# Optimization experiments

Measured on AMD Instinct MI355X. Metric: run time of the kernel, lower is better.

## Reference

```python
import jax, jax.numpy as jnp
import numpy as np

B, T, D, H, F = 4, 2048, 512, 8, 2048
WINDOW = 128
HD = D // H
EPS = 1e-5


def layer_norm(x, g, b):
    mu = jnp.mean(x, axis=-1, keepdims=True)
    var = jnp.mean(jnp.square(x - mu), axis=-1, keepdims=True)
    return (x - mu) * jax.lax.rsqrt(var + EPS) * g + b


def setup_inputs() -> dict:
    key = jax.random.key(0)
    ks = jax.random.split(key, 5)
    s = 0.02
    return {
        "x": jax.random.normal(ks[0], (B, T, D), dtype=jnp.float32),
        "in_proj_w": jax.random.normal(ks[1], (3 * D, D), dtype=jnp.float32) * s,
        "in_proj_b": jnp.zeros((3 * D,), dtype=jnp.float32),
        "out_w": jax.random.normal(ks[2], (D, D), dtype=jnp.float32) * s,
        "out_b": jnp.zeros((D,), dtype=jnp.float32),
        "ln1_g": jnp.ones((D,), dtype=jnp.float32),
        "ln1_b": jnp.zeros((D,), dtype=jnp.float32),
        "ln2_g": jnp.ones((D,), dtype=jnp.float32),
        "ln2_b": jnp.zeros((D,), dtype=jnp.float32),
        "w1": jax.random.normal(ks[3], (F, D), dtype=jnp.float32) * s,
        "b1": jnp.zeros((F,), dtype=jnp.float32),
        "w2": jax.random.normal(ks[4], (D, F), dtype=jnp.float32) * s,
        "b2": jnp.zeros((D,), dtype=jnp.float32),
    }


def reference(x, in_proj_w, in_proj_b, out_w, out_b, ln1_g, ln1_b, ln2_g, ln2_b, w1, b1, w2, b2):
    # pre-norm sliding-window causal self-attention
    x2 = layer_norm(x, ln1_g, ln1_b)
    qkv = x2 @ in_proj_w.T + in_proj_b  # (B,T,3D)
    q, k, v = jnp.split(qkv, 3, axis=-1)
    q = q.reshape(B, T, H, HD)
    k = k.reshape(B, T, H, HD)
    v = v.reshape(B, T, H, HD)
    scale = 1.0 / np.sqrt(HD).astype(np.float32)
    scores = jnp.einsum("bthd,bshd->bhts", q, k) * scale  # dense (B,H,T,T)
    idx = jnp.arange(T)
    i = idx[:, None]
    j = idx[None, :]
    allowed = (j <= i) & (j >= i - WINDOW + 1)  # (T,T) bool, True = attend
    scores = jnp.where(allowed[None, None], scores, -jnp.inf)
    attn = jax.nn.softmax(scores, axis=-1)
    ctx = jnp.einsum("bhts,bshd->bthd", attn, v).reshape(B, T, D)
    attn_out = ctx @ out_w.T + out_b
    x = x + attn_out  # dropout is identity in eval
    # FFN block
    x3 = layer_norm(x, ln2_g, ln2_b)
    h = jax.nn.gelu(x3 @ w1.T + b1, approximate=False)
    x = x + h @ w2.T + b2
    return x
```

## Files before the change

### kernel.cpp

```cpp
#include <hip/hip_runtime.h>
#include <math.h>

constexpr int Bn = 4;
constexpr int Tn = 2048;
constexpr int Dn = 512;
constexpr int Hn = 8;
constexpr int HDn = 64;
constexpr int Fn = 2048;
constexpr int WIN = 128;
constexpr float EPS = 1e-5f;
constexpr int Mrows = Bn * Tn;
constexpr int QKVD = 3 * Dn;

using short8 = __attribute__((ext_vector_type(8))) short;
using f32x4  = __attribute__((ext_vector_type(4))) float;

__device__ __forceinline__ short f2bf(float f) {
    unsigned u = __float_as_uint(f);
    unsigned r = (u + 0x7FFFu + ((u >> 16) & 1u)) >> 16;
    return (short)r;
}

__device__ __forceinline__ float gelu_fast(float v) {
    float u = 1.5957691216f * v * (1.0f + 0.044715f * v * v);
    float t = 1.0f - 2.0f / (__expf(u) + 1.0f);
    return 0.5f * v * (1.0f + t);
}

__device__ __forceinline__ void async16(const short* g, short* l) {
    __builtin_amdgcn_global_load_lds(
        (const __attribute__((address_space(1))) void*)g,
        (__attribute__((address_space(3))) void*)l,
        16, 0, 0);
}

__global__ __launch_bounds__(256) void cvt_all(const float* __restrict__ s0,
                                               const float* __restrict__ s1,
                                               const float* __restrict__ s2,
                                               const float* __restrict__ s3,
                                               short* __restrict__ d0,
                                               short* __restrict__ d1,
                                               short* __restrict__ d2,
                                               short* __restrict__ d3)
{
    int i = blockIdx.x * 256 + threadIdx.x;
    const float* src; short* dst; int j;
    if (i < 196608)      { src = s0; dst = d0; j = i; }
    else if (i < 262144) { src = s1; dst = d1; j = i - 196608; }
    else if (i < 524288) { src = s2; dst = d2; j = i - 262144; }
    else                 { src = s3; dst = d3; j = i - 524288; }
    float4 v = ((const float4*)src)[j];
    short4 o;
    o.x = f2bf(v.x); o.y = f2bf(v.y); o.z = f2bf(v.z); o.w = f2bf(v.w);
    ((short4*)dst)[j] = o;
}

__global__ __launch_bounds__(64) void ln_kernel(const float* __restrict__ x,
                                                const float* __restrict__ g,
                                                const float* __restrict__ b,
                                                short* __restrict__ y)
{
    int row = blockIdx.x;
    int lane = threadIdx.x;
    const float4* xr = (const float4*)(x + (size_t)row * Dn);
    float4 v0 = xr[lane];
    float4 v1 = xr[lane + 64];
    float s = v0.x + v0.y + v0.z + v0.w + v1.x + v1.y + v1.z + v1.w;
#pragma unroll
    for (int off = 32; off >= 1; off >>= 1) s += __shfl_xor(s, off, 64);
    float mu = s * (1.0f / Dn);
    float d0x = v0.x - mu, d0y = v0.y - mu, d0z = v0.z - mu, d0w = v0.w - mu;
    float d1x = v1.x - mu, d1y = v1.y - mu, d1z = v1.z - mu, d1w = v1.w - mu;
    float q = d0x*d0x + d0y*d0y + d0z*d0z + d0w*d0w
            + d1x*d1x + d1y*d1y + d1z*d1z + d1w*d1w;
#pragma unroll
    for (int off = 32; off >= 1; off >>= 1) q += __shfl_xor(q, off, 64);
    float inv = rsqrtf(q * (1.0f / Dn) + EPS);
    const float4* gr = (const float4*)g;
    const float4* br = (const float4*)b;
    float4 g0 = gr[lane], g1 = gr[lane + 64];
    float4 b0 = br[lane], b1 = br[lane + 64];
    short4 a0, a1;
    a0.x = f2bf(d0x * inv * g0.x + b0.x);
    a0.y = f2bf(d0y * inv * g0.y + b0.y);
    a0.z = f2bf(d0z * inv * g0.z + b0.z);
    a0.w = f2bf(d0w * inv * g0.w + b0.w);
    a1.x = f2bf(d1x * inv * g1.x + b1.x);
    a1.y = f2bf(d1y * inv * g1.y + b1.y);
    a1.z = f2bf(d1z * inv * g1.z + b1.z);
    a1.w = f2bf(d1w * inv * g1.w + b1.w);
    short4* yr = (short4*)(y + (size_t)row * Dn);
    yr[lane] = a0;
    yr[lane + 64] = a1;
}

template <int MODE, int BK>
__global__ __launch_bounds__(256) void gemm_mfma(const short* __restrict__ A,
                                                 const short* __restrict__ Bw,
                                                 const float* __restrict__ bias,
                                                 const float* __restrict__ resid,
                                                 void* __restrict__ Cout,
                                                 short* __restrict__ q_out,
                                                 short* __restrict__ k_out,
                                                 short* __restrict__ v_out,
                                                 int M, int N, int K)
{
    constexpr int NCH = BK / 8;
    constexpr int LGN = (BK == 32) ? 2 : 3;
    constexpr int RPI = 512 / BK;
    constexpr int NI  = 32 / RPI;
    constexpr int BUF = 128 * BK;
    constexpr int KK  = BK / 32;
    __shared__ short SMEM[4 * BUF];
    short* Asb = SMEM;
    short* Bsb = SMEM + 2 * BUF;

    int tid = threadIdx.x;
    int w = tid >> 6, lane = tid & 63;
    int wr = w >> 1, wc = w & 1;
    int nN = N >> 7;
    int bid = blockIdx.x;
    int xcd = bid & 7, sq = bid >> 3;
    int mi = xcd + 8 * (sq / nN);
    int ni = sq % nN;
    int m0 = mi * 128, n0 = ni * 128;
    int quad = lane >> 4, l16 = lane & 15;

    f32x4 zero = {0.f, 0.f, 0.f, 0.f};
    f32x4 acc[4][4];
#pragma unroll
    for (int i = 0; i < 4; ++i)
#pragma unroll
        for (int j = 0; j < 4; ++j) acc[i][j] = zero;

    int rl = lane >> LGN;
    int ch = lane & (NCH - 1);
    const short* Ag[NI];
    const short* Bg[NI];
    int ldsOff[NI];
#pragma unroll
    for (int s = 0; s < NI; ++s) {
        int rowl = w * 32 + s * RPI + rl;
        int csw = (ch ^ ((rowl * BK >> 6) & (NCH - 1))) * 8;
        Ag[s] = A + (size_t)(m0 + rowl) * K + csw;
        Bg[s] = Bw + (size_t)(n0 + rowl) * K + csw;
        ldsOff[s] = (w * 32 + s * RPI) * BK;
    }

    auto stage = [&](int kt, int pp) {
#pragma unroll
        for (int s = 0; s < NI; ++s) {
            async16(Ag[s] + kt, Asb + pp * BUF + ldsOff[s]);
            async16(Bg[s] + kt, Bsb + pp * BUF + ldsOff[s]);
        }
    };

    stage(0, 0);
    int p = 0;
    for (int kt = 0; kt < K; kt += BK) {
        __syncthreads();
        if (kt + BK < K) stage(kt + BK, p ^ 1);
        short8 aF[KK][4], bF[KK][4];
#pragma unroll
        for (int kk = 0; kk < KK; ++kk)
#pragma unroll
            for (int i = 0; i < 4; ++i) {
                int ra = wr * 64 + i * 16 + l16;
                int rb = wc * 64 + i * 16 + l16;
                int cs = ((kk * 4 + quad) ^ ((ra * BK >> 6) & (NCH - 1))) * 8;
                aF[kk][i] = *(const short8*)(Asb + p * BUF + ra * BK + cs);
                bF[kk][i] = *(const short8*)(Bsb + p * BUF + rb * BK + cs);
            }
#pragma unroll
        for (int kk = 0; kk < KK; ++kk)
#pragma unroll
            for (int i = 0; i < 4; ++i)
#pragma unroll
                for (int j = 0; j < 4; ++j)
                    acc[i][j] = __builtin_amdgcn_mfma_f32_16x16x32_bf16(
                        aF[kk][i], bF[kk][j], acc[i][j], 0, 0, 0);
        p ^= 1;
    }

    if constexpr (MODE == 3) {
        __syncthreads();
        short* rp = SMEM + w * 2176;
        int b = m0 >> 11;
        int ncol0 = n0 + wc * 64;
        int sec = ncol0 >> 9;
        int h = (ncol0 & 511) >> 6;
        int bh = b * 8 + h;
        int t0 = (m0 & 2047) + wr * 64;
        if (sec == 2) {
#pragma unroll
            for (int ph = 0; ph < 2; ++ph) {
#pragma unroll
                for (int j = 2 * ph; j < 2 * ph + 2; ++j) {
                    int dl = (j - 2 * ph) * 16 + l16;
                    float bv = bias[ncol0 + j * 16 + l16];
#pragma unroll
                    for (int i = 0; i < 4; ++i)
#pragma unroll
                        for (int r = 0; r < 4; ++r)
                            rp[dl * 68 + i * 16 + quad * 4 + r] = f2bf(acc[i][j][r] + bv);
                }
#pragma unroll
                for (int it = 0; it < 4; ++it) {
                    int row = it * 8 + (lane >> 3);
                    int off = (lane & 7) * 8;
                    *(short8*)(v_out + ((size_t)bh * 64 + 32 * ph + row) * 2048 + t0 + off) =
                        *(const short8*)(rp + row * 68 + off);
                }
            }
        } else {
            short* dst = (sec == 0 ? q_out : k_out);
#pragma unroll
            for (int ph = 0; ph < 2; ++ph) {
#pragma unroll
                for (int i = 2 * ph; i < 2 * ph + 2; ++i) {
                    int tl = (i - 2 * ph) * 16 + quad * 4;
#pragma unroll
                    for (int j = 0; j < 4; ++j) {
                        float bv = bias[ncol0 + j * 16 + l16];
#pragma unroll
                        for (int r = 0; r < 4; ++r)
                            rp[(tl + r) * 68 + j * 16 + l16] = f2bf(acc[i][j][r] + bv);
                    }
                }
#pragma unroll
                for (int it = 0; it < 4; ++it) {
                    int row = it * 8 + (lane >> 3);
                    int off = (lane & 7) * 8;
                    *(short8*)(dst + ((size_t)bh * 2048 + t0 + 32 * ph + row) * 64 + off) =
                        *(const short8*)(rp + row * 68 + off);
                }
            }
        }
        return;
    }

    if constexpr (MODE == 2) {
        __syncthreads();
        short* rp = SMEM + w * 2176;
        short* Cb = (short*)Cout;
#pragma unroll
        for (int ph = 0; ph < 2; ++ph) {
#pragma unroll
            for (int i = 2 * ph; i < 2 * ph + 2; ++i) {
                int ml = (i - 2 * ph) * 16 + quad * 4;
#pragma unroll
                for (int j = 0; j < 4; ++j) {
                    float bv = bias[n0 + wc * 64 + j * 16 + l16];
#pragma unroll
                    for (int r = 0; r < 4; ++r)
                        rp[(ml + r) * 68 + j * 16 + l16] =
                            f2bf(gelu_fast(acc[i][j][r] + bv));
                }
            }
#pragma unroll
            for (int it = 0; it < 4; ++it) {
                int row = it * 8 + (lane >> 3);
                int off = (lane & 7) * 8;
                *(short8*)(Cb + (size_t)(m0 + wr * 64 + 32 * ph + row) * N
                              + n0 + wc * 64 + off) =
                    *(const short8*)(rp + row * 68 + off);
            }
        }
        return;
    }

    float* Cf = (float*)Cout;
#pragma unroll
    for (int j = 0; j < 4; ++j) {
        int n = n0 + wc * 64 + j * 16 + l16;
        float bv = bias[n];
#pragma unroll
        for (int i = 0; i < 4; ++i) {
            int mbase = m0 + wr * 64 + i * 16 + quad * 4;
#pragma unroll
            for (int r = 0; r < 4; ++r) {
                size_t idx = (size_t)(mbase + r) * N + n;
                Cf[idx] = acc[i][j][r] + bv + resid[idx];
            }
        }
    }
}

constexpr int QS = 72;
constexpr int VS = 200;

__global__ __launch_bounds__(256) void attn_mfma(const short* __restrict__ Qg,
                                                 const short* __restrict__ Kg,
                                                 const short* __restrict__ Vtg,
                                                 short* __restrict__ ctx)
{
    __shared__ short Qs[64 * QS];
    __shared__ short Ks[192 * QS];
    __shared__ short Vt[64 * VS];
    int tid = threadIdx.x;
    int w = tid >> 6, lane = tid & 63, quad = lane >> 4, l16 = lane & 15;
    int blk = blockIdx.x;
    int q0 = (blk & 31) << 6;
    int bh = blk >> 5;
    int kbase = q0 - 128;

    {
        const short* src = Qg + ((size_t)bh * 2048 + q0) * 64;
        for (int c = tid; c < 512; c += 256) {
            int row = c >> 3, off = (c & 7) * 8;
            *(short8*)(Qs + row * QS + off) = *(const short8*)(src + row * 64 + off);
        }
    }
    {
        const short* base = Kg + (size_t)bh * 2048 * 64;
        for (int c = tid; c < 1536; c += 256) {
            int row = c >> 3, off = (c & 7) * 8;
            int srow = kbase + row; srow = srow < 0 ? 0 : srow;
            *(short8*)(Ks + row * QS + off) = *(const short8*)(base + (size_t)srow * 64 + off);
        }
    }
    {
        const short* base = Vtg + (size_t)bh * 64 * 2048;
        for (int c = tid; c < 1536; c += 256) {
            int row = c / 24, cc = c - row * 24;
            int off = cc * 8;
            int scol = kbase + off; scol = scol < 0 ? 0 : scol;
            *(short8*)(Vt + row * VS + off) = *(const short8*)(base + (size_t)row * 2048 + scol);
        }
    }
    __syncthreads();

    short8 aF0 = *(const short8*)(Qs + (w * 16 + l16) * QS + quad * 8);
    short8 aF1 = *(const short8*)(Qs + (w * 16 + l16) * QS + 32 + quad * 8);
    f32x4 S[12];
    f32x4 zero = {0.f, 0.f, 0.f, 0.f};
#pragma unroll
    for (int t = 0; t < 12; ++t) S[t] = zero;
#pragma unroll
    for (int t = 0; t < 12; ++t) {
        short8 b0 = *(const short8*)(Ks + (t * 16 + l16) * QS + quad * 8);
        short8 b1 = *(const short8*)(Ks + (t * 16 + l16) * QS + 32 + quad * 8);
        S[t] = __builtin_amdgcn_mfma_f32_16x16x32_bf16(aF0, b0, S[t], 0, 0, 0);
        S[t] = __builtin_amdgcn_mfma_f32_16x16x32_bf16(aF1, b1, S[t], 0, 0, 0);
    }

    int i0 = w * 16 + quad * 4;
    float mrow[4] = {-INFINITY, -INFINITY, -INFINITY, -INFINITY};
#pragma unroll
    for (int t = 0; t < 12; ++t) {
        int jl = t * 16 + l16;
        int kg = kbase + jl;
#pragma unroll
        for (int r = 0; r < 4; ++r) {
            int dj = jl - (i0 + r);
            bool ok = (dj >= 1) && (dj <= 128) && (kg >= 0);
            float s = ok ? S[t][r] * 0.125f : -INFINITY;
            S[t][r] = s;
            mrow[r] = fmaxf(mrow[r], s);
        }
    }
#pragma unroll
    for (int off = 8; off >= 1; off >>= 1)
#pragma unroll
        for (int r = 0; r < 4; ++r)
            mrow[r] = fmaxf(mrow[r], __shfl_xor(mrow[r], off, 64));
    float sum[4] = {0.f, 0.f, 0.f, 0.f};
#pragma unroll
    for (int t = 0; t < 12; ++t)
#pragma unroll
        for (int r = 0; r < 4; ++r) {
            float p = __expf(S[t][r] - mrow[r]);
            S[t][r] = p;
            sum[r] += p;
        }
#pragma unroll
    for (int off = 8; off >= 1; off >>= 1)
#pragma unroll
        for (int r = 0; r < 4; ++r)
            sum[r] += __shfl_xor(sum[r], off, 64);
    float inv[4];
#pragma unroll
    for (int r = 0; r < 4; ++r) inv[r] = 1.0f / sum[r];

    __syncthreads();
    short* Ps = Ks;
#pragma unroll
    for (int t = 0; t < 12; ++t)
#pragma unroll
        for (int r = 0; r < 4; ++r)
            Ps[(w * 16 + quad * 4 + r) * VS + t * 16 + l16] = f2bf(S[t][r]);

    f32x4 O[4];
#pragma unroll
    for (int tN = 0; tN < 4; ++tN) O[tN] = zero;
#pragma unroll
    for (int s = 0; s < 6; ++s) {
        short8 aP = *(const short8*)(Ps + (w * 16 + l16) * VS + s * 32 + quad * 8);
#pragma unroll
        for (int tN = 0; tN < 4; ++tN) {
            short8 bV = *(const short8*)(Vt + (tN * 16 + l16) * VS + s * 32 + quad * 8);
            O[tN] = __builtin_amdgcn_mfma_f32_16x16x32_bf16(aP, bV, O[tN], 0, 0, 0);
        }
    }

    int b = bh >> 3, h = bh & 7;
#pragma unroll
    for (int tN = 0; tN < 4; ++tN)
#pragma unroll
        for (int r = 0; r < 4; ++r) {
            int trow = q0 + w * 16 + quad * 4 + r;
            ctx[((size_t)(b * 2048 + trow)) * 512 + h * 64 + tN * 16 + l16] =
                f2bf(O[tN][r] * inv[r]);
        }
}

extern "C" void kernel_launch(void* const* d_in, const int* in_sizes, int n_in,
                              void* d_out, int out_size, void* d_ws, size_t ws_size,
                              hipStream_t stream)
{
    const float* x         = (const float*)d_in[0];
    const float* in_proj_w = (const float*)d_in[1];
    const float* in_proj_b = (const float*)d_in[2];
    const float* out_w     = (const float*)d_in[3];
    const float* out_b     = (const float*)d_in[4];
    const float* ln1_g     = (const float*)d_in[5];
    const float* ln1_b     = (const float*)d_in[6];
    const float* ln2_g     = (const float*)d_in[7];
    const float* ln2_b     = (const float*)d_in[8];
    const float* w1        = (const float*)d_in[9];
    const float* b1        = (const float*)d_in[10];
    const float* w2        = (const float*)d_in[11];
    const float* b2        = (const float*)d_in[12];
    float* out = (float*)d_out;

    char* ws = (char*)d_ws;
    short* attnQ = (short*)ws;
    short* attnK = (short*)(ws + (size_t)8 * 1024 * 1024);
    short* attnV = (short*)(ws + (size_t)16 * 1024 * 1024);
    short* hbuf  = (short*)ws;
    short* regB  = (short*)(ws + (size_t)32 * 1024 * 1024);
    short* wq  = (short*)(ws + (size_t)40 * 1024 * 1024);
    short* wo  = wq + (size_t)QKVD * Dn;
    short* w1b = wo + (size_t)Dn * Dn;
    short* w2b = w1b + (size_t)Fn * Dn;

    cvt_all<<<3072, 256, 0, stream>>>(in_proj_w, out_w, w1, w2, wq, wo, w1b, w2b);

    ln_kernel<<<Mrows, 64, 0, stream>>>(x, ln1_g, ln1_b, regB);
    gemm_mfma<3, 32><<<(Mrows / 128) * (QKVD / 128), 256, 0, stream>>>(
        regB, wq, in_proj_b, nullptr, nullptr, attnQ, attnK, attnV, Mrows, QKVD, Dn);
    attn_mfma<<<Bn * Hn * (Tn / 64), 256, 0, stream>>>(attnQ, attnK, attnV, regB);
    gemm_mfma<1, 64><<<(Mrows / 128) * (Dn / 128), 256, 0, stream>>>(
        regB, wo, out_b, x, out, nullptr, nullptr, nullptr, Mrows, Dn, Dn);
    ln_kernel<<<Mrows, 64, 0, stream>>>(out, ln2_g, ln2_b, regB);
    gemm_mfma<2, 32><<<(Mrows / 128) * (Fn / 128), 256, 0, stream>>>(
        regB, w1b, b1, nullptr, hbuf, nullptr, nullptr, nullptr, Mrows, Fn, Dn);
    gemm_mfma<1, 64><<<(Mrows / 128) * (Dn / 128), 256, 0, stream>>>(
        hbuf, w2b, b2, out, out, nullptr, nullptr, nullptr, Mrows, Dn, Fn);
}
```

Before: 222.2 us.

## Use 128x256 output tiles for QKV and FFN1 GEMMs

Adds a wide GEMM kernel with 128x256 tiles (each wave computes 64x128) for the QKV projection and first FFN GEMM. The residual GEMMs move to a separate specialized 128x128 kernel. Wider tiles raise MFMA work per LDS load and halve the block count, at the cost of more accumulator registers, larger LDS, and fewer blocks in flight. The epilogues are rewritten so that each wave writes two heads for QKV.

Result: faster. 215.9 us (-2.8%).

```diff
diff --git a/kernel.cpp b/kernel.cpp
--- a/kernel.cpp
+++ b/kernel.cpp
@@ -94,23 +94,16 @@
     yr[lane + 64] = a1;
 }
 
-template <int MODE, int BK>
-__global__ __launch_bounds__(256) void gemm_mfma(const short* __restrict__ A,
-                                                 const short* __restrict__ Bw,
-                                                 const float* __restrict__ bias,
-                                                 const float* __restrict__ resid,
-                                                 void* __restrict__ Cout,
-                                                 short* __restrict__ q_out,
-                                                 short* __restrict__ k_out,
-                                                 short* __restrict__ v_out,
-                                                 int M, int N, int K)
+__global__ __launch_bounds__(256) void gemm_res(const short* __restrict__ A,
+                                                const short* __restrict__ Bw,
+                                                const float* __restrict__ bias,
+                                                const float* __restrict__ resid,
+                                                float* __restrict__ Cf,
+                                                int M, int N, int K)
 {
-    constexpr int NCH = BK / 8;
-    constexpr int LGN = (BK == 32) ? 2 : 3;
-    constexpr int RPI = 512 / BK;
-    constexpr int NI  = 32 / RPI;
+    constexpr int BK = 64;
+    constexpr int NCH = 8;
     constexpr int BUF = 128 * BK;
-    constexpr int KK  = BK / 32;
     __shared__ short SMEM[4 * BUF];
     short* Asb = SMEM;
     short* Bsb = SMEM + 2 * BUF;
@@ -133,23 +126,23 @@
 #pragma unroll
         for (int j = 0; j < 4; ++j) acc[i][j] = zero;
 
-    int rl = lane >> LGN;
-    int ch = lane & (NCH - 1);
-    const short* Ag[NI];
-    const short* Bg[NI];
-    int ldsOff[NI];
-#pragma unroll
-    for (int s = 0; s < NI; ++s) {
-        int rowl = w * 32 + s * RPI + rl;
-        int csw = (ch ^ ((rowl * BK >> 6) & (NCH - 1))) * 8;
+    int rl = lane >> 3;
+    int ch = lane & 7;
+    const short* Ag[4];
+    const short* Bg[4];
+    int ldsOff[4];
+#pragma unroll
+    for (int s = 0; s < 4; ++s) {
+        int rowl = w * 32 + s * 8 + rl;
+        int csw = (ch ^ (rowl & 7)) * 8;
         Ag[s] = A + (size_t)(m0 + rowl) * K + csw;
         Bg[s] = Bw + (size_t)(n0 + rowl) * K + csw;
-        ldsOff[s] = (w * 32 + s * RPI) * BK;
+        ldsOff[s] = (w * 32 + s * 8) * BK;
     }
 
     auto stage = [&](int kt, int pp) {
 #pragma unroll
-        for (int s = 0; s < NI; ++s) {
+        for (int s = 0; s < 4; ++s) {
             async16(Ag[s] + kt, Asb + pp * BUF + ldsOff[s]);
             async16(Bg[s] + kt, Bsb + pp * BUF + ldsOff[s]);
         }
@@ -160,19 +153,20 @@
     for (int kt = 0; kt < K; kt += BK) {
         __syncthreads();
         if (kt + BK < K) stage(kt + BK, p ^ 1);
-        short8 aF[KK][4], bF[KK][4];
-#pragma unroll
-        for (int kk = 0; kk < KK; ++kk)
+        short8 aF[2][4], bF[2][4];
+#pragma unroll
+        for (int kk = 0; kk < 2; ++kk)
 #pragma unroll
             for (int i = 0; i < 4; ++i) {
                 int ra = wr * 64 + i * 16 + l16;
                 int rb = wc * 64 + i * 16 + l16;
-                int cs = ((kk * 4 + quad) ^ ((ra * BK >> 6) & (NCH - 1))) * 8;
-                aF[kk][i] = *(const short8*)(Asb + p * BUF + ra * BK + cs);
-                bF[kk][i] = *(const short8*)(Bsb + p * BUF + rb * BK + cs);
+                int csA = ((kk * 4 + quad) ^ (ra & 7)) * 8;
+                int csB = ((kk * 4 + quad) ^ (rb & 7)) * 8;
+                aF[kk][i] = *(const short8*)(Asb + p * BUF + ra * BK + csA);
+                bF[kk][i] = *(const short8*)(Bsb + p * BUF + rb * BK + csB);
             }
 #pragma unroll
-        for (int kk = 0; kk < KK; ++kk)
+        for (int kk = 0; kk < 2; ++kk)
 #pragma unroll
             for (int i = 0; i < 4; ++i)
 #pragma unroll
@@ -182,34 +176,177 @@
         p ^= 1;
     }
 
+#pragma unroll
+    for (int j = 0; j < 4; ++j) {
+        int n = n0 + wc * 64 + j * 16 + l16;
+        float bv = bias[n];
+#pragma unroll
+        for (int i = 0; i < 4; ++i) {
+            int mbase = m0 + wr * 64 + i * 16 + quad * 4;
+#pragma unroll
+            for (int r = 0; r < 4; ++r) {
+                size_t idx = (size_t)(mbase + r) * N + n;
+                Cf[idx] = acc[i][j][r] + bv + resid[idx];
+            }
+        }
+    }
+}
+
+template <int MODE>
+__global__ __launch_bounds__(256, 2) void gemm_wide(const short* __restrict__ A,
+                                                    const short* __restrict__ Bw,
+                                                    const float* __restrict__ bias,
+                                                    void* __restrict__ Cout,
+                                                    short* __restrict__ q_out,
+                                                    short* __restrict__ k_out,
+                                                    short* __restrict__ v_out,
+                                                    int M, int N, int K)
+{
+    constexpr int BK = 32;
+    constexpr int ABUF = 128 * BK;
+    constexpr int BBUF = 256 * BK;
+    __shared__ short SMEM[2 * (ABUF + BBUF)];
+    short* Asb = SMEM;
+    short* Bsb = SMEM + 2 * ABUF;
+
+    int tid = threadIdx.x;
+    int w = tid >> 6, lane = tid & 63;
+    int wr = w >> 1, wc = w & 1;
+    int nT = N >> 8;
+    int bid = blockIdx.x;
+    int xcd = bid & 7, sq = bid >> 3;
+    int mi = xcd + 8 * (sq / nT);
+    int ni = sq % nT;
+    int m0 = mi * 128, n0 = ni * 256;
+    int quad = lane >> 4, l16 = lane & 15;
+
+    f32x4 zero = {0.f, 0.f, 0.f, 0.f};
+    f32x4 acc[4][8];
+#pragma unroll
+    for (int i = 0; i < 4; ++i)
+#pragma unroll
+        for (int j = 0; j < 8; ++j) acc[i][j] = zero;
+
+    int rl = lane >> 2;
+    int ch = lane & 3;
+    const short* Ag[2];
+    const short* Bg[4];
+    int aOff[2], bOff[4];
+#pragma unroll
+    for (int s = 0; s < 2; ++s) {
+        int rowl = w * 32 + s * 16 + rl;
+        int csw = (ch ^ ((rowl >> 1) & 3)) * 8;
+        Ag[s] = A + (size_t)(m0 + rowl) * K + csw;
+        aOff[s] = (w * 32 + s * 16) * BK;
+    }
+#pragma unroll
+    for (int s = 0; s < 4; ++s) {
+        int rowl = w * 64 + s * 16 + rl;
+        int csw = (ch ^ ((rowl >> 1) & 3)) * 8;
+        Bg[s] = Bw + (size_t)(n0 + rowl) * K + csw;
+        bOff[s] = (w * 64 + s * 16) * BK;
+    }
+
+    auto stage = [&](int kt, int pp) {
+#pragma unroll
+        for (int s = 0; s < 2; ++s)
+            async16(Ag[s] + kt, Asb + pp * ABUF + aOff[s]);
+#pragma unroll
+        for (int s = 0; s < 4; ++s)
+            async16(Bg[s] + kt, Bsb + pp * BBUF + bOff[s]);
+    };
+
+    int aoff[4], boff[8];
+#pragma unroll
+    for (int i = 0; i < 4; ++i) {
+        int ra = wr * 64 + i * 16 + l16;
+        aoff[i] = ra * BK + (quad ^ ((ra >> 1) & 3)) * 8;
+    }
+#pragma unroll
+    for (int j = 0; j < 8; ++j) {
+        int rb = wc * 128 + j * 16 + l16;
+        boff[j] = rb * BK + (quad ^ ((rb >> 1) & 3)) * 8;
+    }
+
+    stage(0, 0);
+    int p = 0;
+    for (int kt = 0; kt < K; kt += BK) {
+        __syncthreads();
+        if (kt + BK < K) stage(kt + BK, p ^ 1);
+        short8 aF[4], bF[8];
+#pragma unroll
+        for (int i = 0; i < 4; ++i)
+            aF[i] = *(const short8*)(Asb + p * ABUF + aoff[i]);
+#pragma unroll
+        for (int j = 0; j < 8; ++j)
+            bF[j] = *(const short8*)(Bsb + p * BBUF + boff[j]);
+#pragma unroll
+        for (int i = 0; i < 4; ++i)
+#pragma unroll
+            for (int j = 0; j < 8; ++j)
+                acc[i][j] = __builtin_amdgcn_mfma_f32_16x16x32_bf16(
+                    aF[i], bF[j], acc[i][j], 0, 0, 0);
+        p ^= 1;
+    }
+
+    __syncthreads();
+    short* rp = SMEM + w * 6144;
+    float bv[8];
+#pragma unroll
+    for (int j = 0; j < 8; ++j) bv[j] = bias[n0 + wc * 128 + j * 16 + l16];
+
+    if constexpr (MODE == 2) {
+        short* Cb = (short*)Cout;
+#pragma unroll
+        for (int ph = 0; ph < 2; ++ph) {
+#pragma unroll
+            for (int i = 2 * ph; i < 2 * ph + 2; ++i) {
+                int ml = (i - 2 * ph) * 16 + quad * 4;
+#pragma unroll
+                for (int j = 0; j < 8; ++j)
+#pragma unroll
+                    for (int r = 0; r < 4; ++r)
+                        rp[(ml + r) * 136 + j * 16 + l16] =
+                            f2bf(gelu_fast(acc[i][j][r] + bv[j]));
+            }
+#pragma unroll
+            for (int it = 0; it < 8; ++it) {
+                int row = it * 4 + (lane >> 4);
+                int off = (lane & 15) * 8;
+                *(short8*)(Cb + (size_t)(m0 + wr * 64 + 32 * ph + row) * N
+                              + n0 + wc * 128 + off) =
+                    *(const short8*)(rp + row * 136 + off);
+            }
+        }
+        return;
+    }
+
     if constexpr (MODE == 3) {
-        __syncthreads();
-        short* rp = SMEM + w * 2176;
         int b = m0 >> 11;
-        int ncol0 = n0 + wc * 64;
+        int ncol0 = n0 + wc * 128;
         int sec = ncol0 >> 9;
-        int h = (ncol0 & 511) >> 6;
-        int bh = b * 8 + h;
+        int h0 = (ncol0 & 511) >> 6;
         int t0 = (m0 & 2047) + wr * 64;
         if (sec == 2) {
 #pragma unroll
             for (int ph = 0; ph < 2; ++ph) {
 #pragma unroll
-                for (int j = 2 * ph; j < 2 * ph + 2; ++j) {
-                    int dl = (j - 2 * ph) * 16 + l16;
-                    float bv = bias[ncol0 + j * 16 + l16];
+                for (int j = 4 * ph; j < 4 * ph + 4; ++j) {
+                    int d = (j - 4 * ph) * 16 + l16;
 #pragma unroll
                     for (int i = 0; i < 4; ++i)
 #pragma unroll
                         for (int r = 0; r < 4; ++r)
-                            rp[dl * 68 + i * 16 + quad * 4 + r] = f2bf(acc[i][j][r] + bv);
+                            rp[d * 68 + i * 16 + quad * 4 + r] =
+                                f2bf(acc[i][j][r] + bv[j]);
                 }
-#pragma unroll
-                for (int it = 0; it < 4; ++it) {
-                    int row = it * 8 + (lane >> 3);
+                int bh = b * 8 + h0 + ph;
+#pragma unroll
+                for (int it = 0; it < 8; ++it) {
+                    int drow = it * 8 + (lane >> 3);
                     int off = (lane & 7) * 8;
-                    *(short8*)(v_out + ((size_t)bh * 64 + 32 * ph + row) * 2048 + t0 + off) =
-                        *(const short8*)(rp + row * 68 + off);
+                    *(short8*)(v_out + ((size_t)bh * 64 + drow) * 2048 + t0 + off) =
+                        *(const short8*)(rp + drow * 68 + off);
                 }
             }
         } else {
@@ -220,69 +357,24 @@
                 for (int i = 2 * ph; i < 2 * ph + 2; ++i) {
                     int tl = (i - 2 * ph) * 16 + quad * 4;
 #pragma unroll
-                    for (int j = 0; j < 4; ++j) {
-                        float bv = bias[ncol0 + j * 16 + l16];
+                    for (int j = 0; j < 8; ++j)
 #pragma unroll
                         for (int r = 0; r < 4; ++r)
-                            rp[(tl + r) * 68 + j * 16 + l16] = f2bf(acc[i][j][r] + bv);
-                    }
+                            rp[(tl + r) * 136 + j * 16 + l16] =
+                                f2bf(acc[i][j][r] + bv[j]);
                 }
 #pragma unroll
-                for (int it = 0; it < 4; ++it) {
-                    int row = it * 8 + (lane >> 3);
+                for (int it = 0; it < 8; ++it) {
+                    int trow = it * 4 + (lane >> 4);
+                    int hh = (lane & 15) >> 3;
                     int off = (lane & 7) * 8;
-                    *(short8*)(dst + ((size_t)bh * 2048 + t0 + 32 * ph + row) * 64 + off) =
-                        *(const short8*)(rp + row * 68 + off);
+                    int bh = b * 8 + h0 + hh;
+                    *(short8*)(dst + ((size_t)bh * 2048 + t0 + 32 * ph + trow) * 64 + off) =
+                        *(const short8*)(rp + trow * 136 + hh * 64 + off);
                 }
             }
         }
         return;
-    }
-
-    if constexpr (MODE == 2) {
-        __syncthreads();
-        short* rp = SMEM + w * 2176;
-        short* Cb = (short*)Cout;
-#pragma unroll
-        for (int ph = 0; ph < 2; ++ph) {
-#pragma unroll
-            for (int i = 2 * ph; i < 2 * ph + 2; ++i) {
-                int ml = (i - 2 * ph) * 16 + quad * 4;
-#pragma unroll
-                for (int j = 0; j < 4; ++j) {
-                    float bv = bias[n0 + wc * 64 + j * 16 + l16];
-#pragma unroll
-                    for (int r = 0; r < 4; ++r)
-                        rp[(ml + r) * 68 + j * 16 + l16] =
-                            f2bf(gelu_fast(acc[i][j][r] + bv));
-                }
-            }
-#pragma unroll
-            for (int it = 0; it < 4; ++it) {
-                int row = it * 8 + (lane >> 3);
-                int off = (lane & 7) * 8;
-                *(short8*)(Cb + (size_t)(m0 + wr * 64 + 32 * ph + row) * N
-                              + n0 + wc * 64 + off) =
-                    *(const short8*)(rp + row * 68 + off);
-            }
-        }
-        return;
-    }
-
-    float* Cf = (float*)Cout;
-#pragma unroll
-    for (int j = 0; j < 4; ++j) {
-        int n = n0 + wc * 64 + j * 16 + l16;
-        float bv = bias[n];
-#pragma unroll
-        for (int i = 0; i < 4; ++i) {
-            int mbase = m0 + wr * 64 + i * 16 + quad * 4;
-#pragma unroll
-            for (int r = 0; r < 4; ++r) {
-                size_t idx = (size_t)(mbase + r) * N + n;
-                Cf[idx] = acc[i][j][r] + bv + resid[idx];
-            }
-        }
     }
 }
 
@@ -447,14 +539,14 @@
     cvt_all<<<3072, 256, 0, stream>>>(in_proj_w, out_w, w1, w2, wq, wo, w1b, w2b);
 
     ln_kernel<<<Mrows, 64, 0, stream>>>(x, ln1_g, ln1_b, regB);
-    gemm_mfma<3, 32><<<(Mrows / 128) * (QKVD / 128), 256, 0, stream>>>(
-        regB, wq, in_proj_b, nullptr, nullptr, attnQ, attnK, attnV, Mrows, QKVD, Dn);
+    gemm_wide<3><<<(Mrows / 128) * (QKVD / 256), 256, 0, stream>>>(
+        regB, wq, in_proj_b, nullptr, attnQ, attnK, attnV, Mrows, QKVD, Dn);
     attn_mfma<<<Bn * Hn * (Tn / 64), 256, 0, stream>>>(attnQ, attnK, attnV, regB);
-    gemm_mfma<1, 64><<<(Mrows / 128) * (Dn / 128), 256, 0, stream>>>(
-        regB, wo, out_b, x, out, nullptr, nullptr, nullptr, Mrows, Dn, Dn);
+    gemm_res<<<(Mrows / 128) * (Dn / 128), 256, 0, stream>>>(
+        regB, wo, out_b, x, out, Mrows, Dn, Dn);
     ln_kernel<<<Mrows, 64, 0, stream>>>(out, ln2_g, ln2_b, regB);
-    gemm_mfma<2, 32><<<(Mrows / 128) * (Fn / 128), 256, 0, stream>>>(
-        regB, w1b, b1, nullptr, hbuf, nullptr, nullptr, nullptr, Mrows, Fn, Dn);
-    gemm_mfma<1, 64><<<(Mrows / 128) * (Dn / 128), 256, 0, stream>>>(
-        hbuf, w2b, b2, out, out, nullptr, nullptr, nullptr, Mrows, Dn, Fn);
-}
+    gemm_wide<2><<<(Mrows / 128) * (Fn / 256), 256, 0, stream>>>(
+        regB, w1b, b1, hbuf, nullptr, nullptr, nullptr, Mrows, Fn, Dn);
+    gemm_res<<<(Mrows / 128) * (Dn / 128), 256, 0, stream>>>(
+        hbuf, w2b, b2, out, out, Mrows, Dn, Fn);
+}
```
